# Performance work log

Hardware: AMD Instinct MI355X
Metric: run time of the kernel (lower is better)

Reference implementation:

```python
import jax, jax.numpy as jnp
import numpy as np

BS, DOP, RAN, AZI, ELE = 2, 32, 128, 128, 32
INTERVAL = 0.1
TAU = 1.0


def setup_inputs() -> dict:
    key = jax.random.key(0)
    ks = jax.random.split(key, 7)
    N = RAN * AZI * ELE
    seg = jax.random.normal(ks[0], (BS, N, 1), jnp.float32)
    flow = jax.random.normal(ks[1], (BS, N, 3), jnp.float32) * 2.0
    x1 = jax.random.normal(ks[2], (BS, DOP, RAN, AZI, ELE), jnp.float32)
    dop_arr = jax.random.normal(ks[3], (BS, DOP), jnp.float32)
    coords = jax.random.uniform(ks[4], (BS, 3, RAN, AZI, ELE), jnp.float32)
    ori = jax.random.normal(ks[5], (BS, 3, RAN, AZI, ELE), jnp.float32)
    u = jax.random.uniform(ks[6], (BS, DOP, RAN, AZI, ELE), jnp.float32,
                           minval=1e-6, maxval=1.0 - 1e-6)
    gumbels = -jnp.log(-jnp.log(u))  # Gumbel(0,1) noise (sampled internally in torch)
    return {"seg": seg, "flow": flow, "x1": x1, "dop_arr": dop_arr,
            "coords": coords, "ori": ori, "gumbels": gumbels}


def _gather3d(vol_flat, z, y, x, H, W):
    # vol_flat: (B, C, D*H*W); z,y,x: (B, D, H, W) int32
    B = vol_flat.shape[0]
    idx = ((z * H + y) * W + x).reshape(B, 1, -1)
    g = jnp.take_along_axis(vol_flat, idx, axis=2)
    return g  # (B, C, N)


def _grid_sample_3d_border(vol, gx, gy, gz):
    # Trilinear grid_sample, padding_mode='border', align_corners=True.
    # vol: (B, C, D, H, W); gx/gy/gz: (B, D, H, W) normalized coords in [-1, 1]
    B, C, D, H, W = vol.shape
    ix = jnp.clip((gx + 1.0) * 0.5 * (W - 1), 0.0, W - 1.0)
    iy = jnp.clip((gy + 1.0) * 0.5 * (H - 1), 0.0, H - 1.0)
    iz = jnp.clip((gz + 1.0) * 0.5 * (D - 1), 0.0, D - 1.0)
    x0f, y0f, z0f = jnp.floor(ix), jnp.floor(iy), jnp.floor(iz)
    wx, wy, wz = ix - x0f, iy - y0f, iz - z0f
    x0 = jnp.clip(x0f.astype(jnp.int32), 0, W - 1)
    y0 = jnp.clip(y0f.astype(jnp.int32), 0, H - 1)
    z0 = jnp.clip(z0f.astype(jnp.int32), 0, D - 1)
    x1 = jnp.clip(x0 + 1, 0, W - 1)
    y1 = jnp.clip(y0 + 1, 0, H - 1)
    z1 = jnp.clip(z0 + 1, 0, D - 1)
    vf = vol.reshape(B, C, -1)
    out = jnp.zeros((B, C, D * H * W), vol.dtype)
    for zc, wzc in ((z0, 1.0 - wz), (z1, wz)):
        for yc, wyc in ((y0, 1.0 - wy), (y1, wy)):
            for xc, wxc in ((x0, 1.0 - wx), (x1, wx)):
                w = (wzc * wyc * wxc).reshape(B, 1, -1)
                out = out + w * _gather3d(vf, zc, yc, xc, H, W)
    return out.reshape(B, C, D, H, W)


def _warp_flowxyz(coords, flo):
    B, C, D, H, W = coords.shape
    zz = jnp.arange(D, dtype=jnp.float32)[:, None, None]
    yy = jnp.arange(H, dtype=jnp.float32)[None, :, None]
    xx = jnp.arange(W, dtype=jnp.float32)[None, None, :]
    # vgrid = base grid + flow, per channel (x, y, z)
    vx = xx + flo[:, 0]
    vy = yy + flo[:, 1]
    vz = zz + flo[:, 2]
    gx = 2.0 * vx / (W - 1) - 1.0
    gy = 2.0 * vy / (H - 1) - 1.0
    gz = 2.0 * vz / (D - 1) - 1.0
    r, a, e = coords[:, 0], coords[:, 1], coords[:, 2]
    ce = jnp.cos(e)
    xyz = jnp.stack([r * ce * jnp.cos(a), r * ce * jnp.sin(a), r * jnp.sin(e)], axis=1)
    xyz_new = _grid_sample_3d_border(xyz, gx, gy, gz)
    return xyz_new - xyz


def reference(seg, flow, x1, dop_arr, coords, ori, gumbels):
    bs, dop, ran, azi, ele = x1.shape
    dop_b = dop_arr.reshape(bs, dop, 1, 1, 1)
    # gumbel_softmax(hard=True): forward value is the hard one-hot
    y_soft = jax.nn.softmax((x1 + gumbels) / TAU, axis=1)
    idx = jnp.argmax(y_soft, axis=1)
    y_hard = jax.nn.one_hot(idx, dop, axis=1, dtype=x1.dtype)
    max_x1 = y_hard + y_soft - jax.lax.stop_gradient(y_soft)  # straight-through
    softmax_x1 = jax.nn.softmax(x1, axis=1)
    x1_dop1 = jnp.sum(max_x1 * dop_b, axis=1, keepdims=True)
    x1_dop2 = jnp.sum(softmax_x1 * dop_b, axis=1, keepdims=True)
    x1_dop = jnp.concatenate([x1_dop1, x1_dop2], axis=1)  # (bs, 2, R, A, E)
    seg_v = jnp.transpose(seg, (0, 2, 1)).reshape(bs, -1, ran, azi, ele)
    flow_v = jnp.transpose(flow, (0, 2, 1)).reshape(bs, -1, ran, azi, ele)
    flow_xyz = _warp_flowxyz(coords, flow_v)
    velo = flow_xyz / INTERVAL
    dop_label = jnp.sum(velo * ori, axis=1, keepdims=True)
    dop_error = (dop_label - x1_dop) ** 2
    seg_label = jax.nn.sigmoid(10.0 * (0.15 - dop_error))
    seg_label = jnp.mean(seg_label, axis=1, keepdims=True)
    seg_sig = jax.nn.sigmoid(seg_v)
    loss = jnp.mean(jnp.abs(seg_sig - seg_label))
    return loss
```

## Files before the change

### kernel.cpp

```cpp
#include <hip/hip_runtime.h>
#include <math.h>

#define BSZ  2
#define DOPN 32
#define RAN  128
#define AZI  128
#define ELE  32
#define NVOX (RAN * AZI * ELE)
#define VPT  4
#define TPB  256

__device__ __forceinline__ float sigmoidf_(float t) {
    return 1.0f / (1.0f + __expf(-t));
}

__global__ __launch_bounds__(TPB) void xyz_precompute(
    const float* __restrict__ coords, float* __restrict__ xyz)
{
    const int n0 = (blockIdx.x * TPB + threadIdx.x) * VPT;
    const int b  = blockIdx.y;
    const float* cb = coords + (size_t)b * 3 * NVOX;
    const float4 r4 = *(const float4*)(cb + n0);
    const float4 a4 = *(const float4*)(cb + NVOX + n0);
    const float4 e4 = *(const float4*)(cb + 2 * NVOX + n0);
    const float rr[4] = { r4.x, r4.y, r4.z, r4.w };
    const float aa[4] = { a4.x, a4.y, a4.z, a4.w };
    const float ee[4] = { e4.x, e4.y, e4.z, e4.w };
    float X[4], Y[4], Z[4];
    #pragma unroll
    for (int v = 0; v < VPT; ++v) {
        float sa, ca, se, ce;
        __sincosf(aa[v], &sa, &ca);
        __sincosf(ee[v], &se, &ce);
        X[v] = rr[v] * ce * ca;
        Y[v] = rr[v] * ce * sa;
        Z[v] = rr[v] * se;
    }
    float* xb = xyz + (size_t)b * 3 * NVOX;
    *(float4*)(xb + n0)            = make_float4(X[0], X[1], X[2], X[3]);
    *(float4*)(xb + NVOX + n0)     = make_float4(Y[0], Y[1], Y[2], Y[3]);
    *(float4*)(xb + 2 * NVOX + n0) = make_float4(Z[0], Z[1], Z[2], Z[3]);
}

__global__ __launch_bounds__(TPB) void seg_dop_loss(
    const float* __restrict__ seg, const float* __restrict__ flow,
    const float* __restrict__ x1, const float* __restrict__ dop_arr,
    const float* __restrict__ ori, const float* __restrict__ gumbels,
    const float* __restrict__ xyz, float* __restrict__ out)
{
    __shared__ float s_dop[DOPN];
    __shared__ float s_wave[TPB / 64];

    const int b = blockIdx.y;
    if (threadIdx.x < DOPN) s_dop[threadIdx.x] = dop_arr[b * DOPN + threadIdx.x];
    __syncthreads();

    const int n0 = (blockIdx.x * TPB + threadIdx.x) * VPT;
    const size_t base = (size_t)b * DOPN * NVOX + (size_t)n0;

    float m_lg[VPT] = { -3.4e38f, -3.4e38f, -3.4e38f, -3.4e38f };
    float ssum[VPT] = { 0.f, 0.f, 0.f, 0.f };
    float wsum[VPT] = { 0.f, 0.f, 0.f, 0.f };
    int   idx[VPT]  = { 0, 0, 0, 0 };

    #pragma unroll 4
    for (int d = 0; d < DOPN; ++d) {
        const float4 xv4 = *(const float4*)(x1      + base + (size_t)d * NVOX);
        const float4 gv4 = *(const float4*)(gumbels + base + (size_t)d * NVOX);
        const float dv = s_dop[d];
        const float xv[4] = { xv4.x, xv4.y, xv4.z, xv4.w };
        const float gv[4] = { gv4.x, gv4.y, gv4.z, gv4.w };
        #pragma unroll
        for (int v = 0; v < VPT; ++v) {
            const float lg = xv[v] + gv[v];
            if (lg > m_lg[v]) { m_lg[v] = lg; idx[v] = d; }
            const float ev = __expf(xv[v]);
            ssum[v] += ev;
            wsum[v] += ev * dv;
        }
    }

    const float* fl = flow + ((size_t)b * NVOX + (size_t)n0) * 3;
    float fbuf[12];
    *(float4*)(fbuf)     = *(const float4*)(fl);
    *(float4*)(fbuf + 4) = *(const float4*)(fl + 4);
    *(float4*)(fbuf + 8) = *(const float4*)(fl + 8);

    const float* xb = xyz + (size_t)b * 3 * NVOX;
    const float4 bX4 = *(const float4*)(xb + n0);
    const float4 bY4 = *(const float4*)(xb + NVOX + n0);
    const float4 bZ4 = *(const float4*)(xb + 2 * NVOX + n0);
    const float bX[4] = { bX4.x, bX4.y, bX4.z, bX4.w };
    const float bY[4] = { bY4.x, bY4.y, bY4.z, bY4.w };
    const float bZ[4] = { bZ4.x, bZ4.y, bZ4.z, bZ4.w };

    const float* ob = ori + (size_t)b * 3 * NVOX;
    const float4 oX4 = *(const float4*)(ob + n0);
    const float4 oY4 = *(const float4*)(ob + NVOX + n0);
    const float4 oZ4 = *(const float4*)(ob + 2 * NVOX + n0);
    const float oX[4] = { oX4.x, oX4.y, oX4.z, oX4.w };
    const float oY[4] = { oY4.x, oY4.y, oY4.z, oY4.w };
    const float oZ[4] = { oZ4.x, oZ4.y, oZ4.z, oZ4.w };

    const float4 sg4 = *(const float4*)(seg + (size_t)b * NVOX + n0);
    const float sg[4] = { sg4.x, sg4.y, sg4.z, sg4.w };

    const int xB = n0 & (ELE - 1);
    const int yI = (n0 >> 5) & (AZI - 1);
    const int zI = n0 >> 12;

    float contrib = 0.0f;
    #pragma unroll
    for (int v = 0; v < VPT; ++v) {
        const float vx = (float)(xB + v) + fbuf[3 * v + 0];
        const float vy = (float)yI       + fbuf[3 * v + 1];
        const float vz = (float)zI       + fbuf[3 * v + 2];

        const float gx = 2.0f * vx / (float)(ELE - 1) - 1.0f;
        const float gy = 2.0f * vy / (float)(AZI - 1) - 1.0f;
        const float gz = 2.0f * vz / (float)(RAN - 1) - 1.0f;
        const float ix = fminf(fmaxf((gx + 1.0f) * 0.5f * (float)(ELE - 1), 0.0f), (float)(ELE - 1));
        const float iy = fminf(fmaxf((gy + 1.0f) * 0.5f * (float)(AZI - 1), 0.0f), (float)(AZI - 1));
        const float iz = fminf(fmaxf((gz + 1.0f) * 0.5f * (float)(RAN - 1), 0.0f), (float)(RAN - 1));

        const float x0f = floorf(ix), y0f = floorf(iy), z0f = floorf(iz);
        const float wx = ix - x0f, wy = iy - y0f, wz = iz - z0f;
        int x0 = (int)x0f; x0 = x0 < 0 ? 0 : (x0 > ELE - 1 ? ELE - 1 : x0);
        int y0 = (int)y0f; y0 = y0 < 0 ? 0 : (y0 > AZI - 1 ? AZI - 1 : y0);
        int z0 = (int)z0f; z0 = z0 < 0 ? 0 : (z0 > RAN - 1 ? RAN - 1 : z0);
        const int x1c = x0 + 1 > ELE - 1 ? ELE - 1 : x0 + 1;
        const int y1c = y0 + 1 > AZI - 1 ? AZI - 1 : y0 + 1;
        const int z1c = z0 + 1 > RAN - 1 ? RAN - 1 : z0 + 1;

        const int   zs[2]  = { z0, z1c };
        const int   ys[2]  = { y0, y1c };
        const int   xs[2]  = { x0, x1c };
        const float wzv[2] = { 1.0f - wz, wz };
        const float wyv[2] = { 1.0f - wy, wy };
        const float wxv[2] = { 1.0f - wx, wx };

        float sX = 0.0f, sY = 0.0f, sZ = 0.0f;
        #pragma unroll
        for (int i = 0; i < 2; ++i) {
            #pragma unroll
            for (int j = 0; j < 2; ++j) {
                #pragma unroll
                for (int k = 0; k < 2; ++k) {
                    const float w = wzv[i] * wyv[j] * wxv[k];
                    const int m = (zs[i] * AZI + ys[j]) * ELE + xs[k];
                    sX += w * xb[m];
                    sY += w * xb[NVOX + m];
                    sZ += w * xb[2 * NVOX + m];
                }
            }
        }

        const float vX = (sX - bX[v]) * 10.0f;
        const float vY = (sY - bY[v]) * 10.0f;
        const float vZ = (sZ - bZ[v]) * 10.0f;
        const float dop_label = vX * oX[v] + vY * oY[v] + vZ * oZ[v];

        const float dop1 = s_dop[idx[v]];
        const float dop2 = wsum[v] / ssum[v];
        float e1 = dop_label - dop1; e1 *= e1;
        float e2 = dop_label - dop2; e2 *= e2;
        const float seg_label = 0.5f * (sigmoidf_(10.0f * (0.15f - e1)) +
                                        sigmoidf_(10.0f * (0.15f - e2)));
        contrib += fabsf(sigmoidf_(sg[v]) - seg_label);
    }

    #pragma unroll
    for (int off = 32; off > 0; off >>= 1)
        contrib += __shfl_down(contrib, off, 64);
    const int lane = threadIdx.x & 63;
    const int wid  = threadIdx.x >> 6;
    if (lane == 0) s_wave[wid] = contrib;
    __syncthreads();
    if (threadIdx.x == 0) {
        float bsum = 0.0f;
        #pragma unroll
        for (int w = 0; w < TPB / 64; ++w) bsum += s_wave[w];
        atomicAdd(out, bsum * (1.0f / ((float)BSZ * (float)NVOX)));
    }
}

extern "C" void kernel_launch(void* const* d_in, const int* in_sizes, int n_in,
                              void* d_out, int out_size, void* d_ws, size_t ws_size,
                              hipStream_t stream) {
    const float* seg    = (const float*)d_in[0];
    const float* flow   = (const float*)d_in[1];
    const float* x1     = (const float*)d_in[2];
    const float* dopar  = (const float*)d_in[3];
    const float* coords = (const float*)d_in[4];
    const float* ori    = (const float*)d_in[5];
    const float* gumb   = (const float*)d_in[6];
    float* out = (float*)d_out;
    float* xyz = (float*)d_ws;

    hipMemsetAsync(d_out, 0, sizeof(float) * (size_t)out_size, stream);

    dim3 grid(NVOX / (TPB * VPT), BSZ);
    xyz_precompute<<<grid, TPB, 0, stream>>>(coords, xyz);
    seg_dop_loss<<<grid, TPB, 0, stream>>>(seg, flow, x1, dopar, ori, gumb, xyz, out);
}
```

Measured before the change: 359.1 us.

## Interleave xyz as float4, halve voxels per thread, batch DOP loads

The precomputed Cartesian coordinates are stored interleaved as float4 (AoS), so each trilinear corner needs one 16-byte gather instead of three scattered 4-byte loads. Voxels per thread drop from four to two, which doubles the grid. The 32-channel softmax/argmax loop is split into two halves of 16 channels, with all loads for a half issued up front to raise memory-level parallelism. The cost is a larger xyz workspace carrying a padding lane, narrower float2 streaming loads, and higher register pressure from the 32 preloaded values.

```diff
diff --git a/kernel.cpp b/kernel.cpp
--- a/kernel.cpp
+++ b/kernel.cpp
@@ -7,46 +7,34 @@
 #define AZI  128
 #define ELE  32
 #define NVOX (RAN * AZI * ELE)
-#define VPT  4
 #define TPB  256
+#define VPT  2
+#define DH   16
 
 __device__ __forceinline__ float sigmoidf_(float t) {
     return 1.0f / (1.0f + __expf(-t));
 }
 
 __global__ __launch_bounds__(TPB) void xyz_precompute(
-    const float* __restrict__ coords, float* __restrict__ xyz)
+    const float* __restrict__ coords, float4* __restrict__ xyz4)
 {
-    const int n0 = (blockIdx.x * TPB + threadIdx.x) * VPT;
-    const int b  = blockIdx.y;
+    const int n = blockIdx.x * TPB + threadIdx.x;
+    const int b = blockIdx.y;
     const float* cb = coords + (size_t)b * 3 * NVOX;
-    const float4 r4 = *(const float4*)(cb + n0);
-    const float4 a4 = *(const float4*)(cb + NVOX + n0);
-    const float4 e4 = *(const float4*)(cb + 2 * NVOX + n0);
-    const float rr[4] = { r4.x, r4.y, r4.z, r4.w };
-    const float aa[4] = { a4.x, a4.y, a4.z, a4.w };
-    const float ee[4] = { e4.x, e4.y, e4.z, e4.w };
-    float X[4], Y[4], Z[4];
-    #pragma unroll
-    for (int v = 0; v < VPT; ++v) {
-        float sa, ca, se, ce;
-        __sincosf(aa[v], &sa, &ca);
-        __sincosf(ee[v], &se, &ce);
-        X[v] = rr[v] * ce * ca;
-        Y[v] = rr[v] * ce * sa;
-        Z[v] = rr[v] * se;
-    }
-    float* xb = xyz + (size_t)b * 3 * NVOX;
-    *(float4*)(xb + n0)            = make_float4(X[0], X[1], X[2], X[3]);
-    *(float4*)(xb + NVOX + n0)     = make_float4(Y[0], Y[1], Y[2], Y[3]);
-    *(float4*)(xb + 2 * NVOX + n0) = make_float4(Z[0], Z[1], Z[2], Z[3]);
+    const float r = cb[n];
+    const float a = cb[NVOX + n];
+    const float e = cb[2 * NVOX + n];
+    float sa, ca, se, ce;
+    __sincosf(a, &sa, &ca);
+    __sincosf(e, &se, &ce);
+    xyz4[(size_t)b * NVOX + n] = make_float4(r * ce * ca, r * ce * sa, r * se, 0.0f);
 }
 
 __global__ __launch_bounds__(TPB) void seg_dop_loss(
     const float* __restrict__ seg, const float* __restrict__ flow,
     const float* __restrict__ x1, const float* __restrict__ dop_arr,
     const float* __restrict__ ori, const float* __restrict__ gumbels,
-    const float* __restrict__ xyz, float* __restrict__ out)
+    const float4* __restrict__ xyz4, float* __restrict__ out)
 {
     __shared__ float s_dop[DOPN];
     __shared__ float s_wave[TPB / 64];
@@ -58,52 +46,58 @@
     const int n0 = (blockIdx.x * TPB + threadIdx.x) * VPT;
     const size_t base = (size_t)b * DOPN * NVOX + (size_t)n0;
 
-    float m_lg[VPT] = { -3.4e38f, -3.4e38f, -3.4e38f, -3.4e38f };
-    float ssum[VPT] = { 0.f, 0.f, 0.f, 0.f };
-    float wsum[VPT] = { 0.f, 0.f, 0.f, 0.f };
-    int   idx[VPT]  = { 0, 0, 0, 0 };
-
-    #pragma unroll 4
-    for (int d = 0; d < DOPN; ++d) {
-        const float4 xv4 = *(const float4*)(x1      + base + (size_t)d * NVOX);
-        const float4 gv4 = *(const float4*)(gumbels + base + (size_t)d * NVOX);
-        const float dv = s_dop[d];
-        const float xv[4] = { xv4.x, xv4.y, xv4.z, xv4.w };
-        const float gv[4] = { gv4.x, gv4.y, gv4.z, gv4.w };
-        #pragma unroll
-        for (int v = 0; v < VPT; ++v) {
-            const float lg = xv[v] + gv[v];
-            if (lg > m_lg[v]) { m_lg[v] = lg; idx[v] = d; }
-            const float ev = __expf(xv[v]);
-            ssum[v] += ev;
-            wsum[v] += ev * dv;
+    float m_lg[VPT] = { -3.4e38f, -3.4e38f };
+    float ssum[VPT] = { 0.f, 0.f };
+    float wsum[VPT] = { 0.f, 0.f };
+    int   idx[VPT]  = { 0, 0 };
+
+    for (int h = 0; h < 2; ++h) {
+        const size_t dbase = base + (size_t)h * DH * NVOX;
+        float2 xa[DH], ga[DH];
+        #pragma unroll
+        for (int d = 0; d < DH; ++d)
+            xa[d] = *(const float2*)(x1 + dbase + (size_t)d * NVOX);
+        #pragma unroll
+        for (int d = 0; d < DH; ++d)
+            ga[d] = *(const float2*)(gumbels + dbase + (size_t)d * NVOX);
+        #pragma unroll
+        for (int d = 0; d < DH; ++d) {
+            const int dg = h * DH + d;
+            const float dv = s_dop[dg];
+            const float xv[VPT] = { xa[d].x, xa[d].y };
+            const float gv[VPT] = { ga[d].x, ga[d].y };
+            #pragma unroll
+            for (int v = 0; v < VPT; ++v) {
+                const float lg = xv[v] + gv[v];
+                if (lg > m_lg[v]) { m_lg[v] = lg; idx[v] = dg; }
+                const float ev = __expf(xv[v]);
+                ssum[v] += ev;
+                wsum[v] += ev * dv;
+            }
         }
     }
 
     const float* fl = flow + ((size_t)b * NVOX + (size_t)n0) * 3;
-    float fbuf[12];
-    *(float4*)(fbuf)     = *(const float4*)(fl);
-    *(float4*)(fbuf + 4) = *(const float4*)(fl + 4);
-    *(float4*)(fbuf + 8) = *(const float4*)(fl + 8);
-
-    const float* xb = xyz + (size_t)b * 3 * NVOX;
-    const float4 bX4 = *(const float4*)(xb + n0);
-    const float4 bY4 = *(const float4*)(xb + NVOX + n0);
-    const float4 bZ4 = *(const float4*)(xb + 2 * NVOX + n0);
-    const float bX[4] = { bX4.x, bX4.y, bX4.z, bX4.w };
-    const float bY[4] = { bY4.x, bY4.y, bY4.z, bY4.w };
-    const float bZ[4] = { bZ4.x, bZ4.y, bZ4.z, bZ4.w };
+    float fbuf[3 * VPT];
+    *(float2*)(fbuf)     = *(const float2*)(fl);
+    *(float2*)(fbuf + 2) = *(const float2*)(fl + 2);
+    *(float2*)(fbuf + 4) = *(const float2*)(fl + 4);
+
+    const float4* xb4 = xyz4 + (size_t)b * NVOX;
+    float4 bxyz[VPT];
+    #pragma unroll
+    for (int v = 0; v < VPT; ++v) bxyz[v] = xb4[n0 + v];
 
     const float* ob = ori + (size_t)b * 3 * NVOX;
-    const float4 oX4 = *(const float4*)(ob + n0);
-    const float4 oY4 = *(const float4*)(ob + NVOX + n0);
-    const float4 oZ4 = *(const float4*)(ob + 2 * NVOX + n0);
-    const float oX[4] = { oX4.x, oX4.y, oX4.z, oX4.w };
-    const float oY[4] = { oY4.x, oY4.y, oY4.z, oY4.w };
-    const float oZ[4] = { oZ4.x, oZ4.y, oZ4.z, oZ4.w };
-
-    const float4 sg4 = *(const float4*)(seg + (size_t)b * NVOX + n0);
-    const float sg[4] = { sg4.x, sg4.y, sg4.z, sg4.w };
+    const float2 oX2 = *(const float2*)(ob + n0);
+    const float2 oY2 = *(const float2*)(ob + NVOX + n0);
+    const float2 oZ2 = *(const float2*)(ob + 2 * NVOX + n0);
+    const float oX[VPT] = { oX2.x, oX2.y };
+    const float oY[VPT] = { oY2.x, oY2.y };
+    const float oZ[VPT] = { oZ2.x, oZ2.y };
+
+    const float2 sg2 = *(const float2*)(seg + (size_t)b * NVOX + n0);
+    const float sg[VPT] = { sg2.x, sg2.y };
 
     const int xB = n0 & (ELE - 1);
     const int yI = (n0 >> 5) & (AZI - 1);
@@ -132,32 +126,34 @@
         const int y1c = y0 + 1 > AZI - 1 ? AZI - 1 : y0 + 1;
         const int z1c = z0 + 1 > RAN - 1 ? RAN - 1 : z0 + 1;
 
-        const int   zs[2]  = { z0, z1c };
-        const int   ys[2]  = { y0, y1c };
-        const int   xs[2]  = { x0, x1c };
-        const float wzv[2] = { 1.0f - wz, wz };
-        const float wyv[2] = { 1.0f - wy, wy };
-        const float wxv[2] = { 1.0f - wx, wx };
-
-        float sX = 0.0f, sY = 0.0f, sZ = 0.0f;
-        #pragma unroll
-        for (int i = 0; i < 2; ++i) {
-            #pragma unroll
-            for (int j = 0; j < 2; ++j) {
-                #pragma unroll
-                for (int k = 0; k < 2; ++k) {
-                    const float w = wzv[i] * wyv[j] * wxv[k];
-                    const int m = (zs[i] * AZI + ys[j]) * ELE + xs[k];
-                    sX += w * xb[m];
-                    sY += w * xb[NVOX + m];
-                    sZ += w * xb[2 * NVOX + m];
-                }
-            }
-        }
-
-        const float vX = (sX - bX[v]) * 10.0f;
-        const float vY = (sY - bY[v]) * 10.0f;
-        const float vZ = (sZ - bZ[v]) * 10.0f;
+        const int m00 = (z0  * AZI + y0 ) * ELE;
+        const int m01 = (z0  * AZI + y1c) * ELE;
+        const int m10 = (z1c * AZI + y0 ) * ELE;
+        const int m11 = (z1c * AZI + y1c) * ELE;
+        const float4 c000 = xb4[m00 + x0],  c001 = xb4[m00 + x1c];
+        const float4 c010 = xb4[m01 + x0],  c011 = xb4[m01 + x1c];
+        const float4 c100 = xb4[m10 + x0],  c101 = xb4[m10 + x1c];
+        const float4 c110 = xb4[m11 + x0],  c111 = xb4[m11 + x1c];
+
+        const float w000 = (1.0f - wz) * (1.0f - wy) * (1.0f - wx);
+        const float w001 = (1.0f - wz) * (1.0f - wy) * wx;
+        const float w010 = (1.0f - wz) * wy * (1.0f - wx);
+        const float w011 = (1.0f - wz) * wy * wx;
+        const float w100 = wz * (1.0f - wy) * (1.0f - wx);
+        const float w101 = wz * (1.0f - wy) * wx;
+        const float w110 = wz * wy * (1.0f - wx);
+        const float w111 = wz * wy * wx;
+
+        const float sX = w000*c000.x + w001*c001.x + w010*c010.x + w011*c011.x
+                       + w100*c100.x + w101*c101.x + w110*c110.x + w111*c111.x;
+        const float sY = w000*c000.y + w001*c001.y + w010*c010.y + w011*c011.y
+                       + w100*c100.y + w101*c101.y + w110*c110.y + w111*c111.y;
+        const float sZ = w000*c000.z + w001*c001.z + w010*c010.z + w011*c011.z
+                       + w100*c100.z + w101*c101.z + w110*c110.z + w111*c111.z;
+
+        const float vX = (sX - bxyz[v].x) * 10.0f;
+        const float vY = (sY - bxyz[v].y) * 10.0f;
+        const float vZ = (sZ - bxyz[v].z) * 10.0f;
         const float dop_label = vX * oX[v] + vY * oY[v] + vZ * oZ[v];
 
         const float dop1 = s_dop[idx[v]];
@@ -195,11 +191,12 @@
     const float* ori    = (const float*)d_in[5];
     const float* gumb   = (const float*)d_in[6];
     float* out = (float*)d_out;
-    float* xyz = (float*)d_ws;
+    float4* xyz4 = (float4*)d_ws;
 
     hipMemsetAsync(d_out, 0, sizeof(float) * (size_t)out_size, stream);
 
-    dim3 grid(NVOX / (TPB * VPT), BSZ);
-    xyz_precompute<<<grid, TPB, 0, stream>>>(coords, xyz);
-    seg_dop_loss<<<grid, TPB, 0, stream>>>(seg, flow, x1, dopar, ori, gumb, xyz, out);
-}
+    dim3 gridA(NVOX / TPB, BSZ);
+    xyz_precompute<<<gridA, TPB, 0, stream>>>(coords, xyz4);
+    dim3 gridB(NVOX / (TPB * VPT), BSZ);
+    seg_dop_loss<<<gridB, TPB, 0, stream>>>(seg, flow, x1, dopar, ori, gumb, xyz4, out);
+}
```

New measurement: 325.2 us. 9.4% less time.
